# Performance work log

Hardware: AMD Instinct MI355X
Metric: run time of the kernel (lower is better)

Reference implementation:

```python
import jax, jax.numpy as jnp
import numpy as np

N = 4_000_000
EPS = 1e-6

# Quaternion layout: (w, x, y, z)

def _qmul(q1, q2):
    w1, v1 = q1[..., :1], q1[..., 1:]
    w2, v2 = q2[..., :1], q2[..., 1:]
    w = w1 * w2 - jnp.sum(v1 * v2, axis=-1, keepdims=True)
    v = w1 * v2 + w2 * v1 + jnp.cross(v1, v2)
    return jnp.concatenate([w, v], axis=-1)

def _qinv(q):
    # unit quaternion inverse = conjugate
    return q * jnp.array([1.0, -1.0, -1.0, -1.0], dtype=q.dtype)

def _qlog(q):
    # SO(3) log map: returns tangent vector theta * axis, shape [..., 3]
    w, v = q[..., 0], q[..., 1:]
    nv = jnp.linalg.norm(v, axis=-1)
    small = nv < EPS
    nv_safe = jnp.where(small, 1.0, nv)
    theta = 2.0 * jnp.arctan2(nv, w)
    # small-angle limit: theta/nv -> 2/w
    scale = jnp.where(small, 2.0 / w, theta / nv_safe)
    return v * scale[..., None]

def setup_inputs() -> dict:
    key = jax.random.key(0)
    k1, k2 = jax.random.split(key)
    a = jax.random.normal(k1, (N, 4), dtype=jnp.float32)
    a = a / jnp.linalg.norm(a, axis=-1, keepdims=True)
    idd = jax.random.normal(k2, (N, 4), dtype=jnp.float32)
    idd = idd / jnp.linalg.norm(idd, axis=-1, keepdims=True)
    return {"a": a, "idd": idd}

def reference(a, idd):
    # (a.Inv() @ idd).Log().norm()
    rel = _qmul(_qinv(a), idd)          # [N,4] relative rotation
    tangent = _qlog(rel)                 # [N,3] log map
    return jnp.linalg.norm(tangent)      # scalar Frobenius norm
```

## Files before the change

### kernel.cpp

```cpp
#include <hip/hip_runtime.h>
#include <math.h>

#define BLOCK 256
#define UNROLL 8
#define TILE (BLOCK * UNROLL)

__device__ __forceinline__ float theta_sq(float4 qa, float4 qb) {
    float w1 = qa.x, x1 = -qa.y, y1 = -qa.z, z1 = -qa.w;
    float w2 = qb.x, x2 = qb.y,  y2 = qb.z,  z2 = qb.w;
    float w  = w1*w2 - (x1*x2 + y1*y2 + z1*z2);
    float vx = w1*x2 + w2*x1 + (y1*z2 - z1*y2);
    float vy = w1*y2 + w2*y1 + (z1*x2 - x1*z2);
    float vz = w1*z2 + w2*z1 + (x1*y2 - y1*x2);
    float nv2 = vx*vx + vy*vy + vz*vz;
    if (nv2 < 1e-12f) {
        float s = 2.0f / w;
        return nv2 * s * s;
    }
    float rn = rsqrtf(w*w + nv2);
    float c  = w * rn;
    float ac = fabsf(c);
    float p  = ((-0.0187293f*ac + 0.0742610f)*ac - 0.2121144f)*ac + 1.5707288f;
    float r  = sqrtf(fmaxf(1.0f - ac, 0.0f)) * p;
    float acosc = (c >= 0.0f) ? r : (3.14159265358979f - r);
    float theta = 2.0f * acosc;
    return theta * theta;
}

__global__ __launch_bounds__(BLOCK, 4) void geo_loss_kernel(
        const float4* __restrict__ a,
        const float4* __restrict__ idd,
        float* __restrict__ partials, int n) {
    const int tid  = threadIdx.x;
    const int base = blockIdx.x * TILE + tid;
    float acc = 0.0f;

    if (base + (UNROLL - 1) * BLOCK < n) {
        float4 qa[UNROLL], qb[UNROLL];
        #pragma unroll
        for (int k = 0; k < UNROLL; k++) {
            qa[k] = a[base + k * BLOCK];
            qb[k] = idd[base + k * BLOCK];
        }
        __builtin_amdgcn_sched_barrier(0);
        #pragma unroll
        for (int k = 0; k < UNROLL; k++) acc += theta_sq(qa[k], qb[k]);
    } else {
        for (int k = 0; k < UNROLL; k++) {
            int idx = base + k * BLOCK;
            if (idx < n) acc += theta_sq(a[idx], idd[idx]);
        }
    }

    #pragma unroll
    for (int off = 32; off > 0; off >>= 1)
        acc += __shfl_down(acc, off, 64);
    __shared__ float smem[BLOCK / 64];
    int lane = tid & 63;
    int wid  = tid >> 6;
    if (lane == 0) smem[wid] = acc;
    __syncthreads();
    if (tid == 0) {
        float s = 0.0f;
        #pragma unroll
        for (int i = 0; i < BLOCK / 64; i++) s += smem[i];
        partials[blockIdx.x] = s;
    }
}

__global__ __launch_bounds__(256) void finalize_kernel(
        const float* __restrict__ partials,
        float* __restrict__ out, int nparts) {
    float acc = 0.0f;
    for (int i = threadIdx.x; i < nparts; i += 256)
        acc += partials[i];
    #pragma unroll
    for (int off = 32; off > 0; off >>= 1)
        acc += __shfl_down(acc, off, 64);
    __shared__ float smem[4];
    int lane = threadIdx.x & 63;
    int wid  = threadIdx.x >> 6;
    if (lane == 0) smem[wid] = acc;
    __syncthreads();
    if (threadIdx.x == 0)
        out[0] = sqrtf(smem[0] + smem[1] + smem[2] + smem[3]);
}

extern "C" void kernel_launch(void* const* d_in, const int* in_sizes, int n_in,
                              void* d_out, int out_size, void* d_ws, size_t ws_size,
                              hipStream_t stream) {
    const float4* a   = (const float4*)d_in[0];
    const float4* idd = (const float4*)d_in[1];
    int n = in_sizes[0] / 4;
    float* ws = (float*)d_ws;

    int grid = (n + TILE - 1) / TILE;
    geo_loss_kernel<<<grid, BLOCK, 0, stream>>>(a, idd, ws, n);
    finalize_kernel<<<1, 256, 0, stream>>>(ws, (float*)d_out, grid);
}
```

Measured before the change: 143.4 us.

## Stream tiles through LDS with double-buffered async global_load_lds in persistent grid

Replaces the one-shot register-unrolled loads with a persistent grid of blocks that loop over 512-quaternion tiles. Each tile is prefetched directly into double-buffered LDS with global_load_lds while the previous tile is computed. The goal is to keep memory requests in flight continuously and to reduce the number of blocks launched. In exchange it adds block barriers, manual waitcnt management, and LDS usage that limits occupancy.

```diff
diff --git a/kernel.cpp b/kernel.cpp
--- a/kernel.cpp
+++ b/kernel.cpp
@@ -2,8 +2,9 @@
 #include <math.h>
 
 #define BLOCK 256
-#define UNROLL 8
-#define TILE (BLOCK * UNROLL)
+#define TQ    512
+#define CH    (TQ / BLOCK)
+#define GRID  1280
 
 __device__ __forceinline__ float theta_sq(float4 qa, float4 qb) {
     float w1 = qa.x, x1 = -qa.y, y1 = -qa.z, z1 = -qa.w;
@@ -27,30 +28,55 @@
     return theta * theta;
 }
 
-__global__ __launch_bounds__(BLOCK, 4) void geo_loss_kernel(
+__device__ __forceinline__ void stage_tile(const float4* __restrict__ g,
+                                           float4* lds_arr, int t, int tid) {
+    #pragma unroll
+    for (int c = 0; c < CH; c++) {
+        const float4* gp = g + (size_t)t * TQ + c * BLOCK + tid;
+        float4* lp = lds_arr + c * BLOCK + (tid & ~63);
+        __builtin_amdgcn_global_load_lds(
+            (const __attribute__((address_space(1))) void*)gp,
+            (__attribute__((address_space(3))) void*)lp, 16, 0, 2 );
+    }
+}
+
+__global__ __launch_bounds__(BLOCK) void geo_loss_kernel(
         const float4* __restrict__ a,
         const float4* __restrict__ idd,
-        float* __restrict__ partials, int n) {
-    const int tid  = threadIdx.x;
-    const int base = blockIdx.x * TILE + tid;
+        float* __restrict__ partials, int n, int nfull) {
+    __shared__ float4 ldsbuf[2][2][TQ];
+    const int tid = threadIdx.x;
     float acc = 0.0f;
 
-    if (base + (UNROLL - 1) * BLOCK < n) {
-        float4 qa[UNROLL], qb[UNROLL];
-        #pragma unroll
-        for (int k = 0; k < UNROLL; k++) {
-            qa[k] = a[base + k * BLOCK];
-            qb[k] = idd[base + k * BLOCK];
-        }
-        __builtin_amdgcn_sched_barrier(0);
-        #pragma unroll
-        for (int k = 0; k < UNROLL; k++) acc += theta_sq(qa[k], qb[k]);
-    } else {
-        for (int k = 0; k < UNROLL; k++) {
-            int idx = base + k * BLOCK;
-            if (idx < n) acc += theta_sq(a[idx], idd[idx]);
+    int t = blockIdx.x;
+    int cur = 0;
+    if (t < nfull) {
+        stage_tile(a,   &ldsbuf[0][0][0], t, tid);
+        stage_tile(idd, &ldsbuf[0][1][0], t, tid);
+        for (; t < nfull; t += GRID) {
+            int tn = t + GRID;
+            if (tn < nfull) {
+                stage_tile(a,   &ldsbuf[cur ^ 1][0][0], tn, tid);
+                stage_tile(idd, &ldsbuf[cur ^ 1][1][0], tn, tid);
+                asm volatile("s_waitcnt vmcnt(4)" ::: "memory");
+            } else {
+                asm volatile("s_waitcnt vmcnt(0)" ::: "memory");
+            }
+            __builtin_amdgcn_s_barrier();
+            __builtin_amdgcn_sched_barrier(0);
+            #pragma unroll
+            for (int c = 0; c < CH; c++)
+                acc += theta_sq(ldsbuf[cur][0][c * BLOCK + tid],
+                                ldsbuf[cur][1][c * BLOCK + tid]);
+            asm volatile("s_waitcnt lgkmcnt(0)" ::: "memory");
+            __builtin_amdgcn_s_barrier();
+            cur ^= 1;
         }
     }
+
+    for (int idx = nfull * TQ + blockIdx.x * BLOCK + tid; idx < n;
+         idx += GRID * BLOCK)
+        acc += theta_sq(a[idx], idd[idx]);
 
     #pragma unroll
     for (int off = 32; off > 0; off >>= 1)
@@ -94,7 +120,7 @@
     int n = in_sizes[0] / 4;
     float* ws = (float*)d_ws;
 
-    int grid = (n + TILE - 1) / TILE;
-    geo_loss_kernel<<<grid, BLOCK, 0, stream>>>(a, idd, ws, n);
-    finalize_kernel<<<1, 256, 0, stream>>>(ws, (float*)d_out, grid);
+    int nfull = n / TQ;
+    geo_loss_kernel<<<GRID, BLOCK, 0, stream>>>(a, idd, ws, n, nfull);
+    finalize_kernel<<<1, 256, 0, stream>>>(ws, (float*)d_out, GRID);
 }
```

New measurement: 142.9 us. No clear change (-0.3%).
